# Kernel tuning notes

Measured on AMD Instinct MI355X. Metric: run time of the kernel, lower is better.

## Reference

```python
import jax, jax.numpy as jnp
import numpy as np

B, S, E, H = 2, 2048, 1024, 16
D = E // H
LN_EPS = 1e-5
NORM_EPS = 1e-12  # F.normalize clamp_min


def setup_inputs() -> dict:
    key = jax.random.key(0)
    ks = jax.random.split(key, 4)
    x = jax.random.normal(ks[0], (B, S, E), dtype=jnp.float32)
    qkv_w = jax.random.normal(ks[1], (3 * E, E), dtype=jnp.float32) * 0.02
    qkv_b = jnp.zeros((3 * E,), dtype=jnp.float32)
    out_w = jax.random.normal(ks[2], (E, E), dtype=jnp.float32) * 0.02
    out_b = jnp.zeros((E,), dtype=jnp.float32)
    ln_w = jnp.ones((E,), dtype=jnp.float32)
    ln_b = jnp.zeros((E,), dtype=jnp.float32)
    qknorm_scale = jnp.asarray(E ** -0.5, dtype=jnp.float32)
    # RotaryEmbedding buffer: inv_freq interleaved (emb[::2] = emb[1::2] = base**(-arange(0,E,2)/E))
    base_freq = 10000.0 ** (-(np.arange(0, E, 2).astype(np.float32) / E))
    emb = np.empty((E,), dtype=np.float32)
    emb[::2] = base_freq
    emb[1::2] = base_freq
    inv_freq = jnp.asarray(emb)
    return {"x": x, "ln_w": ln_w, "ln_b": ln_b, "qkv_w": qkv_w, "qkv_b": qkv_b,
            "qknorm_scale": qknorm_scale, "out_w": out_w, "out_b": out_b, "inv_freq": inv_freq}


def _rotate(t, sin, cos):
    # Faithful to source: x1 = even idx (excluding last), x2 = odd idx; cat(-x2, x1)
    x1 = t[..., :-1:2]
    x2 = t[..., 1::2]
    t_rot = jnp.concatenate((-x2, x1), axis=-1)
    return t * cos + t_rot * sin


def _l2norm(t):
    n = jnp.sqrt(jnp.sum(t * t, axis=-1, keepdims=True))
    return t / jnp.maximum(n, NORM_EPS)


def reference(x, ln_w, ln_b, qkv_w, qkv_b, qknorm_scale, out_w, out_b, inv_freq):
    # --- prenorm (LayerNorm, eps=1e-5) ---
    mu = jnp.mean(x, axis=-1, keepdims=True)
    var = jnp.mean((x - mu) ** 2, axis=-1, keepdims=True)
    xn = (x - mu) / jnp.sqrt(var + LN_EPS) * ln_w + ln_b
    # --- QKV projection ---
    qkv = xn @ qkv_w.T + qkv_b  # [B,S,3E]
    q, k, v = jnp.split(qkv, 3, axis=-1)
    # --- rotary (source uses scalar seq*inv_freq, not per-position) ---
    seq = q.shape[1]
    sin = jnp.sin(seq * inv_freq)
    cos = jnp.cos(seq * inv_freq)
    q = _rotate(q, sin, cos)
    k = _rotate(k, sin, cos)
    # --- split heads: [B,S,E] -> [B,H,S,D] ---
    split = lambda t: t.reshape(B, seq, H, D).transpose(0, 2, 1, 3)
    q, k, v = split(q), split(k), split(v)
    # --- qknorm ---
    q = _l2norm(q) * qknorm_scale
    k = _l2norm(k) * qknorm_scale
    # --- scaled dot product with causal mask ---
    aw = jnp.einsum('bhqd,bhkd->bhqk', q, k)  # [B,H,S,S]
    causal = jnp.tril(jnp.ones((seq, seq), dtype=bool))
    aw = jnp.where(causal, aw, jnp.finfo(aw.dtype).min)
    aw = jax.nn.softmax(aw, axis=-1)
    attn = jnp.einsum('bhqk,bhkd->bhqd', aw, v)
    # --- merge heads + out proj ---
    attn = attn.transpose(0, 2, 1, 3).reshape(B, seq, E)
    return attn @ out_w.T + out_b
```

## Files before the change

kernel.cpp:

```cpp
#include <hip/hip_runtime.h>

typedef unsigned short u16;
typedef __attribute__((ext_vector_type(8))) short bf16x8;
typedef __attribute__((ext_vector_type(4))) float f32x4;

#define SS 2048
#define EE 1024
#define HH 16
#define DD 64

__device__ __forceinline__ float b2f(u16 u) {
  union { unsigned int i; float f; } v; v.i = ((unsigned int)u) << 16; return v.f;
}
__device__ __forceinline__ u16 f2b(float f) {
  union { float f; unsigned int i; } v; v.f = f;
  unsigned int i = v.i;
  return (u16)((i + 0x7FFFu + ((i >> 16) & 1u)) >> 16);
}
__device__ __forceinline__ unsigned int cvt_pk_bf16(float lo, float hi) {
  unsigned int r;
  asm("v_cvt_pk_bf16_f32 %0, %1, %2" : "=v"(r) : "v"(lo), "v"(hi));
  return r;
}

#define GLD16(g, l)                                                         \
  __builtin_amdgcn_global_load_lds(                                         \
      (const __attribute__((address_space(1))) unsigned int*)(g),           \
      (__attribute__((address_space(3))) unsigned int*)(l), 16, 0, 0)

__global__ __launch_bounds__(256) void k_prep(const float* __restrict__ qkv_w,
                                              u16* __restrict__ wq_b,
                                              const float* __restrict__ inv_freq,
                                              float2* __restrict__ cs,
                                              const float* __restrict__ x,
                                              const float* __restrict__ lw,
                                              const float* __restrict__ lb,
                                              u16* __restrict__ xn) {
  const int bx = blockIdx.x, t = threadIdx.x;
  if (bx < 3072) {
    const int i = bx * 256 + t;
    float4 v = ((const float4*)qkv_w)[i];
    ushort4 o;
    o.x = f2b(v.x); o.y = f2b(v.y); o.z = f2b(v.z); o.w = f2b(v.w);
    ((ushort4*)wq_b)[i] = o;
    return;
  }
  if (bx < 3076) {
    const int i = (bx - 3072) * 256 + t;
    float th = 2048.0f * inv_freq[i];
    cs[i] = make_float2(cosf(th), sinf(th));
    return;
  }
  const int row = bx - 3076;
  float4 v = ((const float4*)(x + (size_t)row * EE))[t];
  float f0 = v.x, f1 = v.y, f2 = v.z, f3 = v.w;
  float s = f0 + f1 + f2 + f3;
  float ss = f0 * f0 + f1 * f1 + f2 * f2 + f3 * f3;
  for (int o = 1; o < 64; o <<= 1) { s += __shfl_xor(s, o); ss += __shfl_xor(ss, o); }
  __shared__ float red[8];
  int w = t >> 6;
  if ((t & 63) == 0) { red[w] = s; red[4 + w] = ss; }
  __syncthreads();
  s = red[0] + red[1] + red[2] + red[3];
  ss = red[4] + red[5] + red[6] + red[7];
  float mu = s * (1.0f / 1024.0f);
  float var = ss * (1.0f / 1024.0f) - mu * mu;
  float rstd = rsqrtf(var + 1e-5f);
  float4 wv = ((const float4*)lw)[t];
  float4 bv = ((const float4*)lb)[t];
  ushort4 o;
  o.x = f2b((f0 - mu) * rstd * wv.x + bv.x);
  o.y = f2b((f1 - mu) * rstd * wv.y + bv.y);
  o.z = f2b((f2 - mu) * rstd * wv.z + bv.z);
  o.w = f2b((f3 - mu) * rstd * wv.w + bv.w);
  ((ushort4*)(xn + (size_t)row * EE))[t] = o;
}

__global__ __launch_bounds__(256) void k_gemm_b(const u16* __restrict__ A,
                                                const u16* __restrict__ W,
                                                const float* __restrict__ bias,
                                                u16* __restrict__ C,
                                                int M, int N, int K) {
  __shared__ __align__(16) u16 As[128 * 32];
  __shared__ __align__(16) u16 Ws[128 * 32];
  const int t = threadIdx.x;
  const int m0 = blockIdx.y * 128, n0 = blockIdx.x * 128;
  const int lane = t & 63, w = t >> 6, quad = lane >> 4, l15 = lane & 15;
  const int wm = (w & 1) * 64, wn = (w >> 1) * 64;

  f32x4 zero4 = {0.f, 0.f, 0.f, 0.f};
  f32x4 acc[4][4];
  for (int mi = 0; mi < 4; mi++)
    for (int ni = 0; ni < 4; ni++) acc[mi][ni] = zero4;

  const u16* Ag = A + (size_t)(m0 + (t >> 2)) * K + (t & 3) * 8;
  const u16* Wg = W + (size_t)(n0 + (t >> 2)) * K + (t & 3) * 8;
  const size_t rowskip = (size_t)64 * K;

  for (int k0 = 0; k0 < K; k0 += 32) {
    GLD16(Ag + k0, As + t * 8);
    GLD16(Ag + rowskip + k0, As + 2048 + t * 8);
    GLD16(Wg + k0, Ws + t * 8);
    GLD16(Wg + rowskip + k0, Ws + 2048 + t * 8);
    __syncthreads();
    bf16x8 af[4], wf[4];
#pragma unroll
    for (int i = 0; i < 4; i++) {
      af[i] = *(const bf16x8*)(As + (wm + i * 16 + l15) * 32 + quad * 8);
      wf[i] = *(const bf16x8*)(Ws + (wn + i * 16 + l15) * 32 + quad * 8);
    }
#pragma unroll
    for (int mi = 0; mi < 4; mi++)
#pragma unroll
      for (int ni = 0; ni < 4; ni++)
        acc[mi][ni] = __builtin_amdgcn_mfma_f32_16x16x32_bf16(af[mi], wf[ni], acc[mi][ni], 0, 0, 0);
    __syncthreads();
  }
  for (int mi = 0; mi < 4; mi++)
    for (int ni = 0; ni < 4; ni++) {
      int col = n0 + wn + ni * 16 + l15;
      float bb = bias[col];
      for (int r = 0; r < 4; r++) {
        int grow = m0 + wm + mi * 16 + quad * 4 + r;
        C[(size_t)grow * N + col] = f2b(acc[mi][ni][r] + bb);
      }
    }
}

__global__ __launch_bounds__(256) void k_gemm_fw(const u16* __restrict__ A,
                                                 const float* __restrict__ W,
                                                 const float* __restrict__ bias,
                                                 float* __restrict__ C,
                                                 int M, int N, int K) {
  __shared__ __align__(16) u16 As[64 * 32];
  __shared__ __align__(16) u16 Ws[128 * 32];
  const int t = threadIdx.x;
  const int m0 = blockIdx.y * 64, n0 = blockIdx.x * 128;
  const int lane = t & 63, w = t >> 6, quad = lane >> 4, l15 = lane & 15;
  const int wm = (w & 1) * 32, wn = (w >> 1) * 64;

  f32x4 zero4 = {0.f, 0.f, 0.f, 0.f};
  f32x4 acc[2][4];
  for (int mi = 0; mi < 2; mi++)
    for (int ni = 0; ni < 4; ni++) acc[mi][ni] = zero4;

  const u16* Ag = A + (size_t)(m0 + (t >> 2)) * K + (t & 3) * 8;
  const float* Wg0 = W + (size_t)(n0 + (t >> 2)) * K + (t & 3) * 8;
  const float* Wg1 = Wg0 + (size_t)64 * K;

  for (int k0 = 0; k0 < K; k0 += 32) {
    GLD16(Ag + k0, As + t * 8);
    float4 wa = *(const float4*)(Wg0 + k0);
    float4 wb = *(const float4*)(Wg0 + k0 + 4);
    float4 wc = *(const float4*)(Wg1 + k0);
    float4 wd = *(const float4*)(Wg1 + k0 + 4);
    union { unsigned int u[4]; bf16x8 v8; } p0, p1;
    p0.u[0] = cvt_pk_bf16(wa.x, wa.y); p0.u[1] = cvt_pk_bf16(wa.z, wa.w);
    p0.u[2] = cvt_pk_bf16(wb.x, wb.y); p0.u[3] = cvt_pk_bf16(wb.z, wb.w);
    p1.u[0] = cvt_pk_bf16(wc.x, wc.y); p1.u[1] = cvt_pk_bf16(wc.z, wc.w);
    p1.u[2] = cvt_pk_bf16(wd.x, wd.y); p1.u[3] = cvt_pk_bf16(wd.z, wd.w);
    *(bf16x8*)(Ws + t * 8) = p0.v8;
    *(bf16x8*)(Ws + 2048 + t * 8) = p1.v8;
    __syncthreads();
    bf16x8 af[2], wf[4];
#pragma unroll
    for (int i = 0; i < 2; i++)
      af[i] = *(const bf16x8*)(As + (wm + i * 16 + l15) * 32 + quad * 8);
#pragma unroll
    for (int i = 0; i < 4; i++)
      wf[i] = *(const bf16x8*)(Ws + (wn + i * 16 + l15) * 32 + quad * 8);
#pragma unroll
    for (int mi = 0; mi < 2; mi++)
#pragma unroll
      for (int ni = 0; ni < 4; ni++)
        acc[mi][ni] = __builtin_amdgcn_mfma_f32_16x16x32_bf16(af[mi], wf[ni], acc[mi][ni], 0, 0, 0);
    __syncthreads();
  }
  for (int mi = 0; mi < 2; mi++)
    for (int ni = 0; ni < 4; ni++) {
      int col = n0 + wn + ni * 16 + l15;
      float bb = bias[col];
      for (int r = 0; r < 4; r++) {
        int grow = m0 + wm + mi * 16 + quad * 4 + r;
        C[(size_t)grow * N + col] = acc[mi][ni][r] + bb;
      }
    }
}

__global__ __launch_bounds__(256) void k_rotv(u16* __restrict__ qkv,
                                              const float2* __restrict__ cs_tab,
                                              const float* __restrict__ scale_p,
                                              u16* __restrict__ vt) {
  __shared__ float qf[1024];
  __shared__ float kf[1024];
  __shared__ __align__(16) u16 tile[64 * 72];
  const int row = blockIdx.x, t = threadIdx.x;
  {
    u16* qr = qkv + (size_t)row * 3072;
    u16* kr = qr + 1024;
    ushort4 qv = ((const ushort4*)qr)[t];
    ushort4 kv = ((const ushort4*)kr)[t];
    *(float4*)(qf + 4 * t) = make_float4(b2f(qv.x), b2f(qv.y), b2f(qv.z), b2f(qv.w));
    *(float4*)(kf + 4 * t) = make_float4(b2f(kv.x), b2f(kv.y), b2f(kv.z), b2f(kv.w));
    __syncthreads();
    const float scale = scale_p[0];
    float rq[4], rk[4];
#pragma unroll
    for (int u = 0; u < 4; u++) {
      int j = 4 * t + u;
      float2 cs = cs_tab[j];
      float qrot = (j < 512) ? -qf[2 * j + 1] : qf[2 * (j - 512)];
      float krot = (j < 512) ? -kf[2 * j + 1] : kf[2 * (j - 512)];
      rq[u] = qf[j] * cs.x + qrot * cs.y;
      rk[u] = kf[j] * cs.x + krot * cs.y;
    }
    float ssq = rq[0] * rq[0] + rq[1] * rq[1] + rq[2] * rq[2] + rq[3] * rq[3];
    float ssk = rk[0] * rk[0] + rk[1] * rk[1] + rk[2] * rk[2] + rk[3] * rk[3];
    for (int o = 1; o < 16; o <<= 1) { ssq += __shfl_xor(ssq, o); ssk += __shfl_xor(ssk, o); }
    float qs = scale / fmaxf(sqrtf(ssq), 1e-12f);
    float ks = scale / fmaxf(sqrtf(ssk), 1e-12f);
    ushort4 qo, ko;
    qo.x = f2b(rq[0] * qs); qo.y = f2b(rq[1] * qs); qo.z = f2b(rq[2] * qs); qo.w = f2b(rq[3] * qs);
    ko.x = f2b(rk[0] * ks); ko.y = f2b(rk[1] * ks); ko.z = f2b(rk[2] * ks); ko.w = f2b(rk[3] * ks);
    ((ushort4*)qr)[t] = qo;
    ((ushort4*)kr)[t] = ko;
  }
  if (row >= 1024) return;
  const int st = row & 31, bh = row >> 5;
  const int b = bh >> 4, h = bh & 15;
  const int s0 = st * 64;
  const int si = t >> 2, dc = t & 3;
  __syncthreads();
  const u16* src = qkv + (size_t)(b * SS + s0 + si) * 3072 + 2048 + h * DD;
  bf16x8 v0 = *(const bf16x8*)(src + dc * 8);
  bf16x8 v1 = *(const bf16x8*)(src + (dc + 4) * 8);
#pragma unroll
  for (int u = 0; u < 8; u++) tile[(dc * 8 + u) * 72 + si] = (u16)v0[u];
#pragma unroll
  for (int u = 0; u < 8; u++) tile[((dc + 4) * 8 + u) * 72 + si] = (u16)v1[u];
  __syncthreads();
#pragma unroll
  for (int it = 0; it < 2; it++) {
    int idx = t + it * 256;
    int d = idx >> 3, ch = idx & 7;
    bf16x8 o = *(const bf16x8*)(tile + d * 72 + ch * 8);
    *(bf16x8*)(vt + (size_t)(bh * DD + d) * SS + s0 + ch * 8) = o;
  }
}

__global__ __launch_bounds__(512) void k_attn(const u16* __restrict__ qkv,
                                              const u16* __restrict__ vt,
                                              u16* __restrict__ out) {
  __shared__ __align__(16) u16 Kt[128 * 72];
  __shared__ __align__(16) u16 Vt[64 * 136];
  __shared__ __align__(16) u16 Pt[128 * 136];
  const int bh = blockIdx.y;
  const int b = bh >> 4, h = bh & 15;
  const int t = threadIdx.x, w = t >> 6, lane = t & 63, quad = lane >> 4, l15 = lane & 15;
  const int krow = t >> 2, kq = (t & 3) * 16;
  const int dr = t >> 3, kc8 = t & 7;
  const u16* kn = qkv + 1024;
  f32x4 zero4 = {0.f, 0.f, 0.f, 0.f};

  for (int rep = 0; rep < 2; rep++) {
    const int qt = rep ? 15 - (int)blockIdx.x : (int)blockIdx.x;
    const int q0 = qt * 128;

    bf16x8 qf[2];
    {
      const u16* qrow = qkv + (size_t)(b * SS + q0 + 16 * w + l15) * 3072 + h * DD;
      qf[0] = *(const bf16x8*)(qrow + quad * 8);
      qf[1] = *(const bf16x8*)(qrow + 32 + quad * 8);
    }
    f32x4 oacc[4];
    for (int n = 0; n < 4; n++) oacc[n] = zero4;
    float m_i[4] = {-1e30f, -1e30f, -1e30f, -1e30f};
    float l_i[4] = {0.f, 0.f, 0.f, 0.f};

    bf16x8 kv[2], vv[2];
    {
      const u16* krg = kn + (size_t)(b * SS + krow) * 3072 + h * DD + kq;
      kv[0] = *(const bf16x8*)(krg);
      kv[1] = *(const bf16x8*)(krg + 8);
      const u16* vrg = vt + (size_t)(bh * DD + dr) * SS + kc8 * 16;
      vv[0] = *(const bf16x8*)(vrg);
      vv[1] = *(const bf16x8*)(vrg + 8);
    }
    __syncthreads();
    *(bf16x8*)(Kt + krow * 72 + kq) = kv[0];
    *(bf16x8*)(Kt + krow * 72 + kq + 8) = kv[1];
#pragma unroll
    for (int j = 0; j < 2; j++) {
      const int ch = kc8 * 2 + j;
      u16* vb = Vt + dr * 136 + (ch & 1) * 64 + (ch >> 1);
#pragma unroll
      for (int e = 0; e < 8; e++) vb[e * 8] = (u16)vv[j][e];
    }
    __syncthreads();

    for (int kt = 0; kt <= qt; kt++) {
      if (kt < qt) {
        const int k0n = (kt + 1) * 128;
        const u16* krg = kn + (size_t)(b * SS + k0n + krow) * 3072 + h * DD + kq;
        kv[0] = *(const bf16x8*)(krg);
        kv[1] = *(const bf16x8*)(krg + 8);
        const u16* vrg = vt + (size_t)(bh * DD + dr) * SS + k0n + kc8 * 16;
        vv[0] = *(const bf16x8*)(vrg);
        vv[1] = *(const bf16x8*)(vrg + 8);
      }
      f32x4 sacc[8];
#pragma unroll
      for (int n = 0; n < 8; n++) {
        sacc[n] = zero4;
#pragma unroll
        for (int c = 0; c < 2; c++) {
          bf16x8 kfrag = *(const bf16x8*)(Kt + (n * 16 + l15) * 72 + c * 32 + quad * 8);
          sacc[n] = __builtin_amdgcn_mfma_f32_16x16x32_bf16(qf[c], kfrag, sacc[n], 0, 0, 0);
        }
      }
      if (kt == qt) {
        const int rbase = 16 * w + quad * 4;
#pragma unroll
        for (int n = 0; n < 8; n++)
#pragma unroll
          for (int r = 0; r < 4; r++)
            if (n * 16 + l15 > rbase + r) sacc[n][r] = -1e30f;
      }
#pragma unroll
      for (int r = 0; r < 4; r++) {
        float mx = fmaxf(fmaxf(fmaxf(sacc[0][r], sacc[1][r]), fmaxf(sacc[2][r], sacc[3][r])),
                         fmaxf(fmaxf(sacc[4][r], sacc[5][r]), fmaxf(sacc[6][r], sacc[7][r])));
        for (int o = 1; o < 16; o <<= 1) mx = fmaxf(mx, __shfl_xor(mx, o));
        float mn = fmaxf(m_i[r], mx);
        float al = __expf(m_i[r] - mn);
        m_i[r] = mn;
        float rs = 0.f;
#pragma unroll
        for (int n = 0; n < 8; n++) {
          float p = __expf(sacc[n][r] - mn);
          sacc[n][r] = p;
          rs += p;
        }
        for (int o = 1; o < 16; o <<= 1) rs += __shfl_xor(rs, o);
        l_i[r] = al * l_i[r] + rs;
#pragma unroll
        for (int n = 0; n < 4; n++) oacc[n][r] *= al;
      }
#pragma unroll
      for (int r = 0; r < 4; r++) {
        union { unsigned int u[4]; bf16x8 v8; } pk;
        pk.u[0] = cvt_pk_bf16(sacc[0][r], sacc[1][r]);
        pk.u[1] = cvt_pk_bf16(sacc[2][r], sacc[3][r]);
        pk.u[2] = cvt_pk_bf16(sacc[4][r], sacc[5][r]);
        pk.u[3] = cvt_pk_bf16(sacc[6][r], sacc[7][r]);
        *(bf16x8*)(Pt + (16 * w + quad * 4 + r) * 136 + l15 * 8) = pk.v8;
      }
      __syncthreads();
#pragma unroll
      for (int c = 0; c < 4; c++) {
        bf16x8 pf = *(const bf16x8*)(Pt + (16 * w + l15) * 136 + c * 32 + quad * 8);
#pragma unroll
        for (int n = 0; n < 4; n++) {
          bf16x8 vf = *(const bf16x8*)(Vt + (n * 16 + l15) * 136 + c * 32 + quad * 8);
          oacc[n] = __builtin_amdgcn_mfma_f32_16x16x32_bf16(pf, vf, oacc[n], 0, 0, 0);
        }
      }
      __syncthreads();
      if (kt < qt) {
        *(bf16x8*)(Kt + krow * 72 + kq) = kv[0];
        *(bf16x8*)(Kt + krow * 72 + kq + 8) = kv[1];
#pragma unroll
        for (int j = 0; j < 2; j++) {
          const int ch = kc8 * 2 + j;
          u16* vb = Vt + dr * 136 + (ch & 1) * 64 + (ch >> 1);
#pragma unroll
          for (int e = 0; e < 8; e++) vb[e * 8] = (u16)vv[j][e];
        }
      }
      __syncthreads();
    }
    for (int n = 0; n < 4; n++)
      for (int r = 0; r < 4; r++) {
        int row = q0 + 16 * w + quad * 4 + r;
        out[(size_t)(b * SS + row) * EE + h * DD + n * 16 + l15] = f2b(oacc[n][r] / l_i[r]);
      }
  }
}

extern "C" void kernel_launch(void* const* d_in, const int* in_sizes, int n_in,
                              void* d_out, int out_size, void* d_ws, size_t ws_size,
                              hipStream_t stream) {
  const float* x       = (const float*)d_in[0];
  const float* ln_w    = (const float*)d_in[1];
  const float* ln_b    = (const float*)d_in[2];
  const float* qkv_w   = (const float*)d_in[3];
  const float* qkv_b   = (const float*)d_in[4];
  const float* qk_s    = (const float*)d_in[5];
  const float* out_w   = (const float*)d_in[6];
  const float* out_b   = (const float*)d_in[7];
  const float* inv_frq = (const float*)d_in[8];

  u16* ws   = (u16*)d_ws;
  u16* xn   = ws;
  u16* qkv  = ws + (size_t)4096 * 1024;
  u16* wq_b = (u16*)d_out;
  float2* cs_tab = (float2*)((char*)d_out + 6291456);
  u16* vt   = (u16*)d_out + (size_t)4194304;

  k_prep<<<7172, 256, 0, stream>>>(qkv_w, wq_b, inv_frq, cs_tab, x, ln_w, ln_b, xn);
  k_gemm_b<<<dim3(24, 32), 256, 0, stream>>>(xn, wq_b, qkv_b, qkv, 4096, 3072, 1024);
  k_rotv<<<4096, 256, 0, stream>>>(qkv, cs_tab, qk_s, vt);
  k_attn<<<dim3(8, 32), 512, 0, stream>>>(qkv, vt, xn);
  k_gemm_fw<<<dim3(8, 64), 256, 0, stream>>>(xn, out_w, out_b, (float*)d_out, 4096, 1024, 1024);
}
```

Baseline: 231.5 us.

## Compute transposed S tile so softmax rows reduce in-lane and V stores vectorize

Swaps the MFMA operand order so each lane holds one query row with 32 key scores. The row max and sum then need only two cross-lane shuffles instead of sixteen per tile. The P tile is written with 8-byte vector stores, and V is stored to LDS with plain 16-byte stores instead of a scattered per-element transpose. This removes shuffle and LDS scatter overhead, but adds shuffles to redistribute alpha and l back to the output accumulator layout, and changes the LDS ordering of the V/P key dimension, which must stay consistent for correctness.

Result: faster. 219.0 us (-5.4%).

```diff
diff --git a/kernel.cpp b/kernel.cpp
--- a/kernel.cpp
+++ b/kernel.cpp
@@ -259,6 +259,7 @@
   const int t = threadIdx.x, w = t >> 6, lane = t & 63, quad = lane >> 4, l15 = lane & 15;
   const int krow = t >> 2, kq = (t & 3) * 16;
   const int dr = t >> 3, kc8 = t & 7;
+  const int srcl = (lane & 48) + ((lane >> 4) << 2);
   const u16* kn = qkv + 1024;
   f32x4 zero4 = {0.f, 0.f, 0.f, 0.f};
 
@@ -274,8 +275,7 @@
     }
     f32x4 oacc[4];
     for (int n = 0; n < 4; n++) oacc[n] = zero4;
-    float m_i[4] = {-1e30f, -1e30f, -1e30f, -1e30f};
-    float l_i[4] = {0.f, 0.f, 0.f, 0.f};
+    float m_i = -1e30f, l_i = 0.f;
 
     bf16x8 kv[2], vv[2];
     {
@@ -289,13 +289,8 @@
     __syncthreads();
     *(bf16x8*)(Kt + krow * 72 + kq) = kv[0];
     *(bf16x8*)(Kt + krow * 72 + kq + 8) = kv[1];
-#pragma unroll
-    for (int j = 0; j < 2; j++) {
-      const int ch = kc8 * 2 + j;
-      u16* vb = Vt + dr * 136 + (ch & 1) * 64 + (ch >> 1);
-#pragma unroll
-      for (int e = 0; e < 8; e++) vb[e * 8] = (u16)vv[j][e];
-    }
+    *(bf16x8*)(Vt + dr * 136 + kc8 * 16) = vv[0];
+    *(bf16x8*)(Vt + dr * 136 + kc8 * 16 + 8) = vv[1];
     __syncthreads();
 
     for (int kt = 0; kt <= qt; kt++) {
@@ -315,45 +310,52 @@
 #pragma unroll
         for (int c = 0; c < 2; c++) {
           bf16x8 kfrag = *(const bf16x8*)(Kt + (n * 16 + l15) * 72 + c * 32 + quad * 8);
-          sacc[n] = __builtin_amdgcn_mfma_f32_16x16x32_bf16(qf[c], kfrag, sacc[n], 0, 0, 0);
+          sacc[n] = __builtin_amdgcn_mfma_f32_16x16x32_bf16(kfrag, qf[c], sacc[n], 0, 0, 0);
         }
       }
       if (kt == qt) {
-        const int rbase = 16 * w + quad * 4;
+        const int qrow = 16 * w + l15, kbase = 4 * quad;
 #pragma unroll
         for (int n = 0; n < 8; n++)
 #pragma unroll
           for (int r = 0; r < 4; r++)
-            if (n * 16 + l15 > rbase + r) sacc[n][r] = -1e30f;
-      }
-#pragma unroll
-      for (int r = 0; r < 4; r++) {
-        float mx = fmaxf(fmaxf(fmaxf(sacc[0][r], sacc[1][r]), fmaxf(sacc[2][r], sacc[3][r])),
-                         fmaxf(fmaxf(sacc[4][r], sacc[5][r]), fmaxf(sacc[6][r], sacc[7][r])));
-        for (int o = 1; o < 16; o <<= 1) mx = fmaxf(mx, __shfl_xor(mx, o));
-        float mn = fmaxf(m_i[r], mx);
-        float al = __expf(m_i[r] - mn);
-        m_i[r] = mn;
-        float rs = 0.f;
-#pragma unroll
-        for (int n = 0; n < 8; n++) {
+            if (16 * n + kbase + r > qrow) sacc[n][r] = -1e30f;
+      }
+      float mx = -1e30f;
+#pragma unroll
+      for (int n = 0; n < 8; n++)
+#pragma unroll
+        for (int r = 0; r < 4; r++) mx = fmaxf(mx, sacc[n][r]);
+      mx = fmaxf(mx, __shfl_xor(mx, 16));
+      mx = fmaxf(mx, __shfl_xor(mx, 32));
+      float mn = fmaxf(m_i, mx);
+      float al = __expf(m_i - mn);
+      m_i = mn;
+      float rs = 0.f;
+#pragma unroll
+      for (int n = 0; n < 8; n++)
+#pragma unroll
+        for (int r = 0; r < 4; r++) {
           float p = __expf(sacc[n][r] - mn);
           sacc[n][r] = p;
           rs += p;
         }
-        for (int o = 1; o < 16; o <<= 1) rs += __shfl_xor(rs, o);
-        l_i[r] = al * l_i[r] + rs;
-#pragma unroll
-        for (int n = 0; n < 4; n++) oacc[n][r] *= al;
-      }
-#pragma unroll
-      for (int r = 0; r < 4; r++) {
-        union { unsigned int u[4]; bf16x8 v8; } pk;
-        pk.u[0] = cvt_pk_bf16(sacc[0][r], sacc[1][r]);
-        pk.u[1] = cvt_pk_bf16(sacc[2][r], sacc[3][r]);
-        pk.u[2] = cvt_pk_bf16(sacc[4][r], sacc[5][r]);
-        pk.u[3] = cvt_pk_bf16(sacc[6][r], sacc[7][r]);
-        *(bf16x8*)(Pt + (16 * w + quad * 4 + r) * 136 + l15 * 8) = pk.v8;
+      rs += __shfl_xor(rs, 16);
+      rs += __shfl_xor(rs, 32);
+      l_i = al * l_i + rs;
+      float alr[4];
+#pragma unroll
+      for (int r = 0; r < 4; r++) alr[r] = __shfl(al, srcl + r);
+#pragma unroll
+      for (int n = 0; n < 4; n++)
+#pragma unroll
+        for (int r = 0; r < 4; r++) oacc[n][r] *= alr[r];
+#pragma unroll
+      for (int n = 0; n < 8; n++) {
+        uint2 pk;
+        pk.x = cvt_pk_bf16(sacc[n][0], sacc[n][1]);
+        pk.y = cvt_pk_bf16(sacc[n][2], sacc[n][3]);
+        *(uint2*)(Pt + (16 * w + l15) * 136 + 16 * n + 4 * quad) = pk;
       }
       __syncthreads();
 #pragma unroll
@@ -369,20 +371,18 @@
       if (kt < qt) {
         *(bf16x8*)(Kt + krow * 72 + kq) = kv[0];
         *(bf16x8*)(Kt + krow * 72 + kq + 8) = kv[1];
-#pragma unroll
-        for (int j = 0; j < 2; j++) {
-          const int ch = kc8 * 2 + j;
-          u16* vb = Vt + dr * 136 + (ch & 1) * 64 + (ch >> 1);
-#pragma unroll
-          for (int e = 0; e < 8; e++) vb[e * 8] = (u16)vv[j][e];
-        }
+        *(bf16x8*)(Vt + dr * 136 + kc8 * 16) = vv[0];
+        *(bf16x8*)(Vt + dr * 136 + kc8 * 16 + 8) = vv[1];
       }
       __syncthreads();
     }
+    float lr[4];
+#pragma unroll
+    for (int r = 0; r < 4; r++) lr[r] = __shfl(l_i, srcl + r);
     for (int n = 0; n < 4; n++)
       for (int r = 0; r < 4; r++) {
         int row = q0 + 16 * w + quad * 4 + r;
-        out[(size_t)(b * SS + row) * EE + h * DD + n * 16 + l15] = f2b(oacc[n][r] / l_i[r]);
+        out[(size_t)(b * SS + row) * EE + h * DD + n * 16 + l15] = f2b(oacc[n][r] / lr[r]);
       }
   }
 }
```
